# Optimization experiments

Hardware: AMD Instinct MI355X
Metric: run time of the kernel (lower is better)

The kernel has to match this reference:

```python
import jax, jax.numpy as jnp
import numpy as np

B, S, D = 2, 2048, 1024
H, DK, DV = 16, 64, 64


def setup_inputs() -> dict:
    key = jax.random.key(0)
    ks = jax.random.split(key, 10)
    scale = 0.02
    return {
        "x": jax.random.normal(ks[0], (B, S, D), dtype=jnp.float32),
        "Wq": jax.random.normal(ks[1], (D, H * DK), dtype=jnp.float32) * scale,
        "bq": jax.random.normal(ks[2], (H * DK,), dtype=jnp.float32) * scale,
        "Wk": jax.random.normal(ks[3], (D, H * DK), dtype=jnp.float32) * scale,
        "bk": jax.random.normal(ks[4], (H * DK,), dtype=jnp.float32) * scale,
        "Wv": jax.random.normal(ks[5], (D, H * DV), dtype=jnp.float32) * scale,
        "bv": jax.random.normal(ks[6], (H * DV,), dtype=jnp.float32) * scale,
        "Wo": jax.random.normal(ks[7], (H * DV, D), dtype=jnp.float32) * scale,
        "bo": jax.random.normal(ks[8], (D,), dtype=jnp.float32) * scale,
    }


def reference(x, Wq, bq, Wk, bk, Wv, bv, Wo, bo):
    b, s, d = x.shape
    # projections -> (b, H, s, dk/dv)
    q = (x @ Wq + bq).reshape(b, s, H, DK).transpose(0, 2, 1, 3)
    k = (x @ Wk + bk).reshape(b, s, H, DK).transpose(0, 2, 1, 3)
    v = (x @ Wv + bv).reshape(b, s, H, DV).transpose(0, 2, 1, 3)
    # scaled QK^T: (b, H, s, s)
    scores = jnp.einsum("bhqd,bhkd->bhqk", q, k) / np.sqrt(DK).astype(np.float32)
    # sign-based reweighting: scores * sign(scores) (zeros -> sign 1) == |scores|
    reweighted = jnp.abs(scores)
    # causal mask: lower triangle keeps value, strict upper -> -inf (value * -inf)
    causal = jnp.tril(jnp.ones((s, s), dtype=bool))
    logits = jnp.where(causal, reweighted, -jnp.inf)
    w = jax.nn.softmax(logits, axis=-1)
    o = jnp.einsum("bhqk,bhkd->bhqd", w, v)  # (b, H, s, DV)
    o = o.transpose(0, 2, 1, 3).reshape(b, s, H * DV)
    return o @ Wo + bo
```

## Files before the change

### kernel.cpp

```cpp
#include <hip/hip_runtime.h>


#define DI __device__ __forceinline__

typedef __bf16 bf16x8 __attribute__((ext_vector_type(8)));
typedef float f32x4 __attribute__((ext_vector_type(4)));
typedef unsigned short u16x8 __attribute__((ext_vector_type(8)));
typedef unsigned short u16x4 __attribute__((ext_vector_type(4)));

union U8 { u16x8 u; bf16x8 b; };
union PB { unsigned int w[4]; u16x8 u; bf16x8 b; };

typedef const __attribute__((address_space(1))) unsigned int* gas_p;
typedef __attribute__((address_space(3))) unsigned int* las_p;

DI void gload16(const unsigned short* g, unsigned short* l) {
  __builtin_amdgcn_global_load_lds((gas_p)(const void*)g, (las_p)(void*)l, 16, 0, 0);
}

#define WAIT_VM4  asm volatile("s_waitcnt vmcnt(4)" ::: "memory")
#define WAIT_VM0  asm volatile("s_waitcnt vmcnt(0)" ::: "memory")
#define WAIT_LGKM asm volatile("s_waitcnt lgkmcnt(0)" ::: "memory")
#define BARRIER   __builtin_amdgcn_s_barrier()

DI unsigned short f2bf(float f) {
  unsigned int u = __float_as_uint(f);
  u += 0x7FFFu + ((u >> 16) & 1u);
  return (unsigned short)(u >> 16);
}

__global__ __launch_bounds__(256) void k_conv_x(const float* __restrict__ x,
                                                unsigned short* __restrict__ xb) {
  size_t i = ((size_t)blockIdx.x * 256 + threadIdx.x) * 4;
  float4 v = *(const float4*)(x + i);
  u16x4 o;
  o[0] = f2bf(v.x); o[1] = f2bf(v.y); o[2] = f2bf(v.z); o[3] = f2bf(v.w);
  *(u16x4*)(xb + i) = o;
}

__global__ __launch_bounds__(256) void k_transpose(
    const float* __restrict__ W0, const float* __restrict__ W1,
    const float* __restrict__ W2, const float* __restrict__ W3,
    unsigned short* __restrict__ T0, unsigned short* __restrict__ T1,
    unsigned short* __restrict__ T2, unsigned short* __restrict__ T3) {
  const int z = blockIdx.z;
  const float* W = (z == 0) ? W0 : (z == 1) ? W1 : (z == 2) ? W2 : W3;
  unsigned short* T = (z == 0) ? T0 : (z == 1) ? T1 : (z == 2) ? T2 : T3;
  __shared__ unsigned short buf[32][33];
  const int k0 = blockIdx.x * 32, n0 = blockIdx.y * 32;
  const int tx = threadIdx.x, ty = threadIdx.y;
#pragma unroll
  for (int j = 0; j < 4; ++j) {
    int r = ty + j * 8;
    buf[r][tx] = f2bf(W[(size_t)(k0 + r) * 1024 + n0 + tx]);
  }
  __syncthreads();
#pragma unroll
  for (int j = 0; j < 4; ++j) {
    int c = ty + j * 8;
    T[(size_t)(n0 + c) * 1024 + k0 + tx] = buf[tx][c];
  }
}

DI void stage_gemm(const unsigned short* __restrict__ src, unsigned short* dst,
                   int row0, int k0, int tid, int wid) {
#pragma unroll
  for (int i = 0; i < 2; ++i) {
    int T = i * 256 + tid;
    int row = T >> 2, ch = T & 3;
    int sch = ch ^ (row & 3);
    gload16(&src[(size_t)(row0 + row) * 1024 + k0 + sch * 8],
            &dst[(i * 256 + wid * 64) * 8]);
  }
}

DI void gemm_main(const unsigned short* __restrict__ A,
                  const unsigned short* __restrict__ Bm,
                  unsigned short* As, unsigned short* Bs,
                  int m0, int n0, f32x4 acc[4][4]) {
  const int tid = threadIdx.x;
  const int lane = tid & 63, wid = tid >> 6;
  const int wr = wid >> 1, wc = wid & 1;
  const int g = lane >> 4, lq = lane & 15;

  stage_gemm(A, As, m0, 0, tid, wid);
  stage_gemm(Bm, Bs, n0, 0, tid, wid);
  __syncthreads();
  int buf = 0;
  for (int k0 = 0; k0 < 1024; k0 += 32) {
    if (k0 + 32 < 1024) {
      stage_gemm(A, As + (buf ^ 1) * 4096, m0, k0 + 32, tid, wid);
      stage_gemm(Bm, Bs + (buf ^ 1) * 4096, n0, k0 + 32, tid, wid);
    }
    const unsigned short* Ab = As + buf * 4096;
    const unsigned short* Bb = Bs + buf * 4096;
    U8 af[4], bfr[4];
#pragma unroll
    for (int f = 0; f < 4; ++f) {
      af[f].u  = *(const u16x8*)&Ab[(wr * 64 + f * 16 + lq) * 32 + ((g ^ (lq & 3)) * 8)];
      bfr[f].u = *(const u16x8*)&Bb[(wc * 64 + f * 16 + lq) * 32 + ((g ^ (lq & 3)) * 8)];
    }
#pragma unroll
    for (int i = 0; i < 4; ++i)
#pragma unroll
      for (int j = 0; j < 4; ++j)
        acc[i][j] = __builtin_amdgcn_mfma_f32_16x16x32_bf16(af[i].b, bfr[j].b,
                                                            acc[i][j], 0, 0, 0);
    __syncthreads();
    buf ^= 1;
  }
}

__global__ __launch_bounds__(256) void k_gemm_qkv(
    const unsigned short* __restrict__ xb,
    const unsigned short* __restrict__ Wqt, const unsigned short* __restrict__ Wkt,
    const unsigned short* __restrict__ Wvt,
    const float* __restrict__ bq, const float* __restrict__ bk,
    const float* __restrict__ bv,
    unsigned short* __restrict__ Qo, unsigned short* __restrict__ Ko,
    unsigned short* __restrict__ Vto) {
  __shared__ unsigned short As[2 * 4096];
  __shared__ unsigned short Bs[2 * 4096];
  const int z = blockIdx.z;
  const unsigned short* Bm = (z == 0) ? Wqt : (z == 1) ? Wkt : Wvt;
  const float* bias = (z == 0) ? bq : (z == 1) ? bk : bv;

  f32x4 acc[4][4];
#pragma unroll
  for (int i = 0; i < 4; ++i)
#pragma unroll
    for (int j = 0; j < 4; ++j) acc[i][j] = f32x4{0.f, 0.f, 0.f, 0.f};

  const int m0 = blockIdx.x * 128, n0 = blockIdx.y * 128;
  gemm_main(xb, Bm, As, Bs, m0, n0, acc);

  const int lane = threadIdx.x & 63, wid = threadIdx.x >> 6;
  const int wr = wid >> 1, wc = wid & 1;
  const int g = lane >> 4, lq = lane & 15;
  unsigned short* dstQK = (z == 0) ? Qo : Ko;
#pragma unroll
  for (int j = 0; j < 4; ++j) {
    int col = n0 + wc * 64 + j * 16 + lq;
    float bv_ = bias[col];
    int h = col >> 6, d = col & 63;
#pragma unroll
    for (int i = 0; i < 4; ++i) {
#pragma unroll
      for (int r = 0; r < 4; ++r) {
        int row = m0 + wr * 64 + i * 16 + g * 4 + r;
        int b = row >> 11, s = row & 2047;
        unsigned short hv = f2bf(acc[i][j][r] + bv_);
        if (z < 2)
          dstQK[(((size_t)(b * 16 + h)) * 2048 + s) * 64 + d] = hv;
        else
          Vto[(((size_t)(b * 16 + h)) * 64 + d) * 2048 + s] = hv;
      }
    }
  }
}

__global__ __launch_bounds__(256) void k_gemm_out(
    const unsigned short* __restrict__ Ob, const unsigned short* __restrict__ Wot,
    const float* __restrict__ bo, float* __restrict__ out) {
  __shared__ unsigned short As[2 * 4096];
  __shared__ unsigned short Bs[2 * 4096];
  f32x4 acc[4][4];
#pragma unroll
  for (int i = 0; i < 4; ++i)
#pragma unroll
    for (int j = 0; j < 4; ++j) acc[i][j] = f32x4{0.f, 0.f, 0.f, 0.f};

  const int m0 = blockIdx.x * 128, n0 = blockIdx.y * 128;
  gemm_main(Ob, Wot, As, Bs, m0, n0, acc);

  const int lane = threadIdx.x & 63, wid = threadIdx.x >> 6;
  const int wr = wid >> 1, wc = wid & 1;
  const int g = lane >> 4, lq = lane & 15;
#pragma unroll
  for (int j = 0; j < 4; ++j) {
    int col = n0 + wc * 64 + j * 16 + lq;
    float bv_ = bo[col];
#pragma unroll
    for (int i = 0; i < 4; ++i)
#pragma unroll
      for (int r = 0; r < 4; ++r) {
        int row = m0 + wr * 64 + i * 16 + g * 4 + r;
        out[(size_t)row * 1024 + col] = acc[i][j][r] + bv_;
      }
  }
}

template<bool MASKED>
DI void ptile(f32x4 sacc[4], f32x4& lacc, unsigned int pk[4][2], int qloc, int g) {
  const float SC = 0.18033688011112042f;
#pragma unroll
  for (int c = 0; c < 4; ++c) {
#pragma unroll
    for (int r = 0; r < 4; ++r) {
      float sv = fabsf(sacc[c][r]) * SC;
      if (MASKED) {
        int k = c * 16 + g * 4 + r;
        sv = (k <= qloc) ? sv : -1e30f;
      }
      float p = exp2f(sv);
      sacc[c][r] = p;
      lacc[r] += p;
    }
    asm("v_cvt_pk_bf16_f32 %0, %1, %2"
        : "=v"(pk[c][0]) : "v"(sacc[c][0]), "v"(sacc[c][1]));
    asm("v_cvt_pk_bf16_f32 %0, %1, %2"
        : "=v"(pk[c][1]) : "v"(sacc[c][2]), "v"(sacc[c][3]));
  }
}

__global__ __launch_bounds__(256) void k_flash(
    const unsigned short* __restrict__ Q, const unsigned short* __restrict__ Km,
    const unsigned short* __restrict__ Vt, unsigned short* __restrict__ O) {
  const int tid = threadIdx.x;
  const int lane = tid & 63, wid = tid >> 6;
  const int g = lane >> 4, lq = lane & 15;
  const int bid = blockIdx.x;
  const int xcd = bid & 7, idx = bid >> 3;
  const int bh = xcd * 4 + (idx >> 4);
  const int pairidx = idx & 15;
  const int b = bh >> 4, h = bh & 15;
  const size_t qkbase = (size_t)bh * 2048 * 64;
  const size_t vbase = (size_t)bh * 64 * 2048;
  const int qloc = wid * 16 + lq;

  __shared__ unsigned short Ks[2][64 * 64];
  __shared__ unsigned short Vs[2][64 * 64];

  auto stage = [&](int bf, int t) {
    const int kk0 = t * 64;
#pragma unroll
    for (int i = 0; i < 2; ++i) {
      int T = i * 256 + tid;
      int row = T >> 3, ch = T & 7;
      int sch = ch ^ (row & 7);
      gload16(&Km[qkbase + (size_t)(kk0 + row) * 64 + sch * 8],
              &Ks[bf][(i * 2048 + wid * 512)]);
      gload16(&Vt[vbase + (size_t)row * 2048 + kk0 + sch * 8],
              &Vs[bf][(i * 2048 + wid * 512)]);
    }
  };

  for (int ph = 0; ph < 2; ++ph) {
    const int qb = ph ? (31 - pairidx) : pairidx;
    const int q0 = qb * 64;
    const int qrow = q0 + qloc;

    U8 aq0, aq1;
    {
      const unsigned short* qp = &Q[qkbase + (size_t)qrow * 64 + g * 8];
      aq0.u = *(const u16x8*)qp;
      aq1.u = *(const u16x8*)(qp + 32);
    }
    f32x4 lacc = f32x4{0.f, 0.f, 0.f, 0.f};
    f32x4 oacc[4];
#pragma unroll
    for (int c = 0; c < 4; ++c) oacc[c] = f32x4{0.f, 0.f, 0.f, 0.f};

    const int nt = qb + 1;
    stage(0, 0);
    if (nt > 1) stage(1, 1);
    int buf = 0;
    for (int t = 0; t < nt; ++t) {
      if (t + 1 < nt) WAIT_VM4; else WAIT_VM0;
      BARRIER;
      f32x4 sacc[4];
      __builtin_amdgcn_s_setprio(1);
#pragma unroll
      for (int c = 0; c < 4; ++c) {
        U8 kf0, kf1;
        kf0.u = *(const u16x8*)&Ks[buf][(c * 16 + lq) * 64 + (((0 * 4 + g) ^ (lq & 7)) * 8)];
        kf1.u = *(const u16x8*)&Ks[buf][(c * 16 + lq) * 64 + (((1 * 4 + g) ^ (lq & 7)) * 8)];
        sacc[c] = __builtin_amdgcn_mfma_f32_16x16x32_bf16(kf0.b, aq0.b,
                                                          f32x4{0.f, 0.f, 0.f, 0.f}, 0, 0, 0);
        sacc[c] = __builtin_amdgcn_mfma_f32_16x16x32_bf16(kf1.b, aq1.b, sacc[c], 0, 0, 0);
      }
      __builtin_amdgcn_s_setprio(0);
      unsigned int pk[4][2];
      if (t == nt - 1) ptile<true>(sacc, lacc, pk, qloc, g);
      else            ptile<false>(sacc, lacc, pk, qloc, g);
      __builtin_amdgcn_s_setprio(1);
#pragma unroll
      for (int hh = 0; hh < 2; ++hh) {
        PB pb;
#pragma unroll
        for (int w2 = 0; w2 < 4; ++w2) {
          int src = (((g & 1) * 2 + (w2 >> 1)) << 4) + lq;
          unsigned int lo = __shfl(pk[hh * 2 + 0][w2 & 1], src, 64);
          unsigned int hi = __shfl(pk[hh * 2 + 1][w2 & 1], src, 64);
          pb.w[w2] = (g >> 1) ? hi : lo;
        }
#pragma unroll
        for (int c = 0; c < 4; ++c) {
          U8 vf;
          vf.u = *(const u16x8*)&Vs[buf][(c * 16 + lq) * 64 + (((hh * 4 + g) ^ (lq & 7)) * 8)];
          oacc[c] = __builtin_amdgcn_mfma_f32_16x16x32_bf16(vf.b, pb.b, oacc[c], 0, 0, 0);
        }
      }
      __builtin_amdgcn_s_setprio(0);
      WAIT_LGKM;
      BARRIER;
      if (t + 2 < nt) stage(buf, t + 2);
      buf ^= 1;
    }
    float lsum = (lacc[0] + lacc[1]) + (lacc[2] + lacc[3]);
    lsum += __shfl_xor(lsum, 16, 64);
    lsum += __shfl_xor(lsum, 32, 64);
    float inv_l = 1.0f / lsum;
#pragma unroll
    for (int c = 0; c < 4; ++c) {
      u16x4 ov;
#pragma unroll
      for (int r = 0; r < 4; ++r) ov[r] = f2bf(oacc[c][r] * inv_l);
      *(u16x4*)&O[((size_t)(b * 2048 + qrow)) * 1024 + h * 64 + c * 16 + g * 4] = ov;
    }
  }
}

extern "C" void kernel_launch(void* const* d_in, const int* in_sizes, int n_in,
                              void* d_out, int out_size, void* d_ws, size_t ws_size,
                              hipStream_t stream) {
  const float* x  = (const float*)d_in[0];
  const float* Wq = (const float*)d_in[1];
  const float* bq = (const float*)d_in[2];
  const float* Wk = (const float*)d_in[3];
  const float* bk = (const float*)d_in[4];
  const float* Wv = (const float*)d_in[5];
  const float* bv = (const float*)d_in[6];
  const float* Wo = (const float*)d_in[7];
  const float* bo = (const float*)d_in[8];
  float* out = (float*)d_out;

  char* ws = (char*)d_ws;
  const size_t MB = 1024 * 1024;
  unsigned short* xb   = (unsigned short*)(ws + 0 * MB);
  unsigned short* Wqt  = (unsigned short*)(ws + 8 * MB);
  unsigned short* Wkt  = (unsigned short*)(ws + 10 * MB);
  unsigned short* Wvt  = (unsigned short*)(ws + 12 * MB);
  unsigned short* Wot  = (unsigned short*)(ws + 14 * MB);
  unsigned short* Qws  = (unsigned short*)(ws + 16 * MB);
  unsigned short* Kws  = (unsigned short*)(ws + 24 * MB);
  unsigned short* Vtws = (unsigned short*)(ws + 32 * MB);
  unsigned short* Ows  = (unsigned short*)(ws + 40 * MB);

  k_conv_x<<<4096, 256, 0, stream>>>(x, xb);
  k_transpose<<<dim3(32, 32, 4), dim3(32, 8), 0, stream>>>(Wq, Wk, Wv, Wo,
                                                           Wqt, Wkt, Wvt, Wot);
  k_gemm_qkv<<<dim3(32, 8, 3), 256, 0, stream>>>(xb, Wqt, Wkt, Wvt, bq, bk, bv,
                                                 Qws, Kws, Vtws);
  k_flash<<<512, 256, 0, stream>>>(Qws, Kws, Vtws, Ows);
  k_gemm_out<<<dim3(32, 8), 256, 0, stream>>>(Ows, Wot, bo, out);
}
```

Measured before the change: 126.5 us.

## Split long causal query blocks across two CTAs and stage QKV epilogue through LDS

The flash kernel now launches twice as many blocks. Each pair of blocks shares the work of a short and a long query block: the long block's key range is split in two, each half writes unnormalized bf16 partial outputs and row sums to workspace, and a new combine kernel merges them. This is meant to balance work per block and raise occupancy, at the cost of an extra launch, extra global traffic and bf16 rounding of the partials. Separately, the QKV GEMM epilogue now writes the tile into shared memory first, then does coalesced 16-byte stores for Q/K and the transposed V, replacing the scattered 2-byte stores.

```diff
diff --git a/kernel.cpp b/kernel.cpp
--- a/kernel.cpp
+++ b/kernel.cpp
@@ -28,6 +28,7 @@
   u += 0x7FFFu + ((u >> 16) & 1u);
   return (unsigned short)(u >> 16);
 }
+DI float bf2f(unsigned short v) { return __uint_as_float((unsigned int)v << 16); }
 
 __global__ __launch_bounds__(256) void k_conv_x(const float* __restrict__ x,
                                                 unsigned short* __restrict__ xb) {
@@ -119,8 +120,9 @@
     const float* __restrict__ bv,
     unsigned short* __restrict__ Qo, unsigned short* __restrict__ Ko,
     unsigned short* __restrict__ Vto) {
-  __shared__ unsigned short As[2 * 4096];
-  __shared__ unsigned short Bs[2 * 4096];
+  __shared__ unsigned short Sh[128 * 136];
+  unsigned short* As = Sh;
+  unsigned short* Bs = Sh + 8192;
   const int z = blockIdx.z;
   const unsigned short* Bm = (z == 0) ? Wqt : (z == 1) ? Wkt : Wvt;
   const float* bias = (z == 0) ? bq : (z == 1) ? bk : bv;
@@ -134,27 +136,50 @@
   const int m0 = blockIdx.x * 128, n0 = blockIdx.y * 128;
   gemm_main(xb, Bm, As, Bs, m0, n0, acc);
 
-  const int lane = threadIdx.x & 63, wid = threadIdx.x >> 6;
+  const int tid = threadIdx.x;
+  const int lane = tid & 63, wid = tid >> 6;
   const int wr = wid >> 1, wc = wid & 1;
   const int g = lane >> 4, lq = lane & 15;
-  unsigned short* dstQK = (z == 0) ? Qo : Ko;
+  const int bb = m0 >> 11;
+
 #pragma unroll
   for (int j = 0; j < 4; ++j) {
-    int col = n0 + wc * 64 + j * 16 + lq;
-    float bv_ = bias[col];
-    int h = col >> 6, d = col & 63;
-#pragma unroll
-    for (int i = 0; i < 4; ++i) {
+    int col = wc * 64 + j * 16 + lq;
+    float bv_ = bias[n0 + col];
+#pragma unroll
+    for (int i = 0; i < 4; ++i)
 #pragma unroll
       for (int r = 0; r < 4; ++r) {
-        int row = m0 + wr * 64 + i * 16 + g * 4 + r;
-        int b = row >> 11, s = row & 2047;
-        unsigned short hv = f2bf(acc[i][j][r] + bv_);
-        if (z < 2)
-          dstQK[(((size_t)(b * 16 + h)) * 2048 + s) * 64 + d] = hv;
-        else
-          Vto[(((size_t)(b * 16 + h)) * 64 + d) * 2048 + s] = hv;
-      }
+        int row = wr * 64 + i * 16 + g * 4 + r;
+        Sh[row * 136 + col] = f2bf(acc[i][j][r] + bv_);
+      }
+  }
+  __syncthreads();
+
+  if (z < 2) {
+    unsigned short* dstQK = (z == 0) ? Qo : Ko;
+    const int ch = tid & 15, sb = tid >> 4;
+#pragma unroll
+    for (int it = 0; it < 8; ++it) {
+      int s = sb + it * 16;
+      u16x8 v = *(const u16x8*)&Sh[s * 136 + ch * 8];
+      int gcol = n0 + ch * 8;
+      int hh = gcol >> 6, dd = gcol & 63;
+      int sr = (m0 + s) & 2047;
+      *(u16x8*)&dstQK[(((size_t)(bb * 16 + hh)) * 2048 + sr) * 64 + dd] = v;
+    }
+  } else {
+    const int d = tid & 127, hf = tid >> 7;
+    int gcol = n0 + d;
+    int hh = gcol >> 6, dd = gcol & 63;
+    size_t vrow = ((size_t)(bb * 16 + hh)) * 64 + dd;
+#pragma unroll
+    for (int it = 0; it < 8; ++it) {
+      int s0 = (hf + it * 2) * 8;
+      u16x8 vv;
+#pragma unroll
+      for (int e = 0; e < 8; ++e) vv[e] = Sh[(s0 + e) * 136 + d];
+      *(u16x8*)&Vto[vrow * 2048 + (m0 & 2047) + s0] = vv;
     }
   }
 }
@@ -213,20 +238,29 @@
   }
 }
 
-__global__ __launch_bounds__(256) void k_flash(
+__global__ __launch_bounds__(256, 4) void k_flash(
     const unsigned short* __restrict__ Q, const unsigned short* __restrict__ Km,
-    const unsigned short* __restrict__ Vt, unsigned short* __restrict__ O) {
+    const unsigned short* __restrict__ Vt, unsigned short* __restrict__ O,
+    unsigned short* __restrict__ Pp, float* __restrict__ Lp) {
   const int tid = threadIdx.x;
   const int lane = tid & 63, wid = tid >> 6;
   const int g = lane >> 4, lq = lane & 15;
   const int bid = blockIdx.x;
-  const int xcd = bid & 7, idx = bid >> 3;
-  const int bh = xcd * 4 + (idx >> 4);
-  const int pairidx = idx & 15;
+  const int xcd = bid & 7, r = bid >> 3;
+  const int bh = xcd * 4 + (r >> 5);
+  const int rr = r & 31;
+  const int p = rr >> 1, sp = rr & 1;
   const int b = bh >> 4, h = bh & 15;
   const size_t qkbase = (size_t)bh * 2048 * 64;
   const size_t vbase = (size_t)bh * 64 * 2048;
   const int qloc = wid * 16 + lq;
+
+  const int ntA = p + 1;
+  const int mq = 31 - p, mi = 15 - p;
+  const bool hasA = (sp == 0);
+  int t0, t1, limB;
+  if (sp == 0) { int u = 16 - p; t0 = 0; t1 = (ntA > u) ? ntA : u; limB = u; }
+  else         { t0 = 16 - p; t1 = 32 - p; limB = 1 << 30; }
 
   __shared__ unsigned short Ks[2][64 * 64];
   __shared__ unsigned short Vs[2][64 * 64];
@@ -245,80 +279,147 @@
     }
   };
 
-  for (int ph = 0; ph < 2; ++ph) {
-    const int qb = ph ? (31 - pairidx) : pairidx;
-    const int q0 = qb * 64;
-    const int qrow = q0 + qloc;
-
-    U8 aq0, aq1;
-    {
-      const unsigned short* qp = &Q[qkbase + (size_t)qrow * 64 + g * 8];
-      aq0.u = *(const u16x8*)qp;
-      aq1.u = *(const u16x8*)(qp + 32);
-    }
-    f32x4 lacc = f32x4{0.f, 0.f, 0.f, 0.f};
-    f32x4 oacc[4];
-#pragma unroll
-    for (int c = 0; c < 4; ++c) oacc[c] = f32x4{0.f, 0.f, 0.f, 0.f};
-
-    const int nt = qb + 1;
-    stage(0, 0);
-    if (nt > 1) stage(1, 1);
-    int buf = 0;
-    for (int t = 0; t < nt; ++t) {
-      if (t + 1 < nt) WAIT_VM4; else WAIT_VM0;
-      BARRIER;
-      f32x4 sacc[4];
-      __builtin_amdgcn_s_setprio(1);
+  U8 aqA0, aqA1, aqB0, aqB1;
+  if (hasA) {
+    const unsigned short* qp = &Q[qkbase + (size_t)(p * 64 + qloc) * 64 + g * 8];
+    aqA0.u = *(const u16x8*)qp;
+    aqA1.u = *(const u16x8*)(qp + 32);
+  }
+  {
+    const unsigned short* qp = &Q[qkbase + (size_t)(mq * 64 + qloc) * 64 + g * 8];
+    aqB0.u = *(const u16x8*)qp;
+    aqB1.u = *(const u16x8*)(qp + 32);
+  }
+  f32x4 laccA = f32x4{0.f, 0.f, 0.f, 0.f}, laccB = f32x4{0.f, 0.f, 0.f, 0.f};
+  f32x4 oaccA[4], oaccB[4];
+#pragma unroll
+  for (int c = 0; c < 4; ++c) {
+    oaccA[c] = f32x4{0.f, 0.f, 0.f, 0.f};
+    oaccB[c] = f32x4{0.f, 0.f, 0.f, 0.f};
+  }
+
+  stage(0, t0);
+  stage(1, t0 + 1);
+  int buf = 0;
+  for (int t = t0; t < t1; ++t) {
+    if (t + 1 < t1) WAIT_VM4; else WAIT_VM0;
+    BARRIER;
+    const bool condA = hasA && (t < ntA);
+    const bool condB = (t < limB);
+    f32x4 saccA[4], saccB[4];
+    __builtin_amdgcn_s_setprio(1);
+#pragma unroll
+    for (int c = 0; c < 4; ++c) {
+      U8 kf0, kf1;
+      kf0.u = *(const u16x8*)&Ks[buf][(c * 16 + lq) * 64 + (((0 * 4 + g) ^ (lq & 7)) * 8)];
+      kf1.u = *(const u16x8*)&Ks[buf][(c * 16 + lq) * 64 + (((1 * 4 + g) ^ (lq & 7)) * 8)];
+      if (condA) {
+        saccA[c] = __builtin_amdgcn_mfma_f32_16x16x32_bf16(kf0.b, aqA0.b,
+                                                           f32x4{0.f, 0.f, 0.f, 0.f}, 0, 0, 0);
+        saccA[c] = __builtin_amdgcn_mfma_f32_16x16x32_bf16(kf1.b, aqA1.b, saccA[c], 0, 0, 0);
+      }
+      if (condB) {
+        saccB[c] = __builtin_amdgcn_mfma_f32_16x16x32_bf16(kf0.b, aqB0.b,
+                                                           f32x4{0.f, 0.f, 0.f, 0.f}, 0, 0, 0);
+        saccB[c] = __builtin_amdgcn_mfma_f32_16x16x32_bf16(kf1.b, aqB1.b, saccB[c], 0, 0, 0);
+      }
+    }
+    __builtin_amdgcn_s_setprio(0);
+    unsigned int pkA[4][2], pkB[4][2];
+    if (condA) {
+      if (t == p) ptile<true>(saccA, laccA, pkA, qloc, g);
+      else        ptile<false>(saccA, laccA, pkA, qloc, g);
+    }
+    if (condB) {
+      if (t == mq) ptile<true>(saccB, laccB, pkB, qloc, g);
+      else         ptile<false>(saccB, laccB, pkB, qloc, g);
+    }
+    __builtin_amdgcn_s_setprio(1);
+#pragma unroll
+    for (int hh = 0; hh < 2; ++hh) {
+      PB pbA, pbB;
+#pragma unroll
+      for (int w2 = 0; w2 < 4; ++w2) {
+        int src = (((g & 1) * 2 + (w2 >> 1)) << 4) + lq;
+        if (condA) {
+          unsigned int lo = __shfl(pkA[hh * 2 + 0][w2 & 1], src, 64);
+          unsigned int hi = __shfl(pkA[hh * 2 + 1][w2 & 1], src, 64);
+          pbA.w[w2] = (g >> 1) ? hi : lo;
+        }
+        if (condB) {
+          unsigned int lo = __shfl(pkB[hh * 2 + 0][w2 & 1], src, 64);
+          unsigned int hi = __shfl(pkB[hh * 2 + 1][w2 & 1], src, 64);
+          pbB.w[w2] = (g >> 1) ? hi : lo;
+        }
+      }
 #pragma unroll
       for (int c = 0; c < 4; ++c) {
-        U8 kf0, kf1;
-        kf0.u = *(const u16x8*)&Ks[buf][(c * 16 + lq) * 64 + (((0 * 4 + g) ^ (lq & 7)) * 8)];
-        kf1.u = *(const u16x8*)&Ks[buf][(c * 16 + lq) * 64 + (((1 * 4 + g) ^ (lq & 7)) * 8)];
-        sacc[c] = __builtin_amdgcn_mfma_f32_16x16x32_bf16(kf0.b, aq0.b,
-                                                          f32x4{0.f, 0.f, 0.f, 0.f}, 0, 0, 0);
-        sacc[c] = __builtin_amdgcn_mfma_f32_16x16x32_bf16(kf1.b, aq1.b, sacc[c], 0, 0, 0);
-      }
-      __builtin_amdgcn_s_setprio(0);
-      unsigned int pk[4][2];
-      if (t == nt - 1) ptile<true>(sacc, lacc, pk, qloc, g);
-      else            ptile<false>(sacc, lacc, pk, qloc, g);
-      __builtin_amdgcn_s_setprio(1);
-#pragma unroll
-      for (int hh = 0; hh < 2; ++hh) {
-        PB pb;
-#pragma unroll
-        for (int w2 = 0; w2 < 4; ++w2) {
-          int src = (((g & 1) * 2 + (w2 >> 1)) << 4) + lq;
-          unsigned int lo = __shfl(pk[hh * 2 + 0][w2 & 1], src, 64);
-          unsigned int hi = __shfl(pk[hh * 2 + 1][w2 & 1], src, 64);
-          pb.w[w2] = (g >> 1) ? hi : lo;
-        }
-#pragma unroll
-        for (int c = 0; c < 4; ++c) {
-          U8 vf;
-          vf.u = *(const u16x8*)&Vs[buf][(c * 16 + lq) * 64 + (((hh * 4 + g) ^ (lq & 7)) * 8)];
-          oacc[c] = __builtin_amdgcn_mfma_f32_16x16x32_bf16(vf.b, pb.b, oacc[c], 0, 0, 0);
-        }
-      }
-      __builtin_amdgcn_s_setprio(0);
-      WAIT_LGKM;
-      BARRIER;
-      if (t + 2 < nt) stage(buf, t + 2);
-      buf ^= 1;
-    }
-    float lsum = (lacc[0] + lacc[1]) + (lacc[2] + lacc[3]);
-    lsum += __shfl_xor(lsum, 16, 64);
-    lsum += __shfl_xor(lsum, 32, 64);
-    float inv_l = 1.0f / lsum;
+        U8 vf;
+        vf.u = *(const u16x8*)&Vs[buf][(c * 16 + lq) * 64 + (((hh * 4 + g) ^ (lq & 7)) * 8)];
+        if (condA)
+          oaccA[c] = __builtin_amdgcn_mfma_f32_16x16x32_bf16(vf.b, pbA.b, oaccA[c], 0, 0, 0);
+        if (condB)
+          oaccB[c] = __builtin_amdgcn_mfma_f32_16x16x32_bf16(vf.b, pbB.b, oaccB[c], 0, 0, 0);
+      }
+    }
+    __builtin_amdgcn_s_setprio(0);
+    WAIT_LGKM;
+    BARRIER;
+    if (t + 2 < t1) stage(buf, t + 2);
+    buf ^= 1;
+  }
+
+  if (hasA) {
+    float ls = (laccA[0] + laccA[1]) + (laccA[2] + laccA[3]);
+    ls += __shfl_xor(ls, 16, 64);
+    ls += __shfl_xor(ls, 32, 64);
+    float inv_l = 1.0f / ls;
+    int qrow = p * 64 + qloc;
 #pragma unroll
     for (int c = 0; c < 4; ++c) {
       u16x4 ov;
 #pragma unroll
-      for (int r = 0; r < 4; ++r) ov[r] = f2bf(oacc[c][r] * inv_l);
+      for (int r2 = 0; r2 < 4; ++r2) ov[r2] = f2bf(oaccA[c][r2] * inv_l);
       *(u16x4*)&O[((size_t)(b * 2048 + qrow)) * 1024 + h * 64 + c * 16 + g * 4] = ov;
     }
   }
+  {
+    float ls = (laccB[0] + laccB[1]) + (laccB[2] + laccB[3]);
+    ls += __shfl_xor(ls, 16, 64);
+    ls += __shfl_xor(ls, 32, 64);
+    int slot = (bh * 16 + mi) * 2 + sp;
+    if (g == 0) Lp[slot * 64 + qloc] = ls;
+    size_t pbase = (size_t)slot * 4096 + qloc * 64;
+#pragma unroll
+    for (int c = 0; c < 4; ++c) {
+      u16x4 ov;
+#pragma unroll
+      for (int r2 = 0; r2 < 4; ++r2) ov[r2] = f2bf(oaccB[c][r2]);
+      *(u16x4*)&Pp[pbase + c * 16 + g * 4] = ov;
+    }
+  }
+}
+
+__global__ __launch_bounds__(256) void k_combine(
+    const unsigned short* __restrict__ Pp, const float* __restrict__ Lp,
+    unsigned short* __restrict__ O) {
+  int gid = blockIdx.x * 256 + threadIdx.x;
+  int dv4 = gid & 15;
+  int q   = (gid >> 4) & 63;
+  int mi  = (gid >> 10) & 15;
+  int bh  = gid >> 14;
+  int pairbase = (bh * 16 + mi) * 2;
+  size_t base = (size_t)pairbase * 4096 + q * 64 + dv4 * 4;
+  u16x4 a = *(const u16x4*)&Pp[base];
+  u16x4 c = *(const u16x4*)&Pp[base + 4096];
+  float l = Lp[pairbase * 64 + q] + Lp[(pairbase + 1) * 64 + q];
+  float inv = 1.0f / l;
+  u16x4 o;
+#pragma unroll
+  for (int r = 0; r < 4; ++r) o[r] = f2bf((bf2f(a[r]) + bf2f(c[r])) * inv);
+  int b = bh >> 4, h = bh & 15;
+  int srow = (mi + 16) * 64 + q;
+  *(u16x4*)&O[((size_t)(b * 2048 + srow)) * 1024 + h * 64 + dv4 * 4] = o;
 }
 
 extern "C" void kernel_launch(void* const* d_in, const int* in_sizes, int n_in,
@@ -346,12 +447,15 @@
   unsigned short* Kws  = (unsigned short*)(ws + 24 * MB);
   unsigned short* Vtws = (unsigned short*)(ws + 32 * MB);
   unsigned short* Ows  = (unsigned short*)(ws + 40 * MB);
+  unsigned short* Pp   = (unsigned short*)(ws + 0 * MB);
+  float*          Lp   = (float*)(ws + 8 * MB);
 
   k_conv_x<<<4096, 256, 0, stream>>>(x, xb);
   k_transpose<<<dim3(32, 32, 4), dim3(32, 8), 0, stream>>>(Wq, Wk, Wv, Wo,
                                                            Wqt, Wkt, Wvt, Wot);
   k_gemm_qkv<<<dim3(32, 8, 3), 256, 0, stream>>>(xb, Wqt, Wkt, Wvt, bq, bk, bv,
                                                  Qws, Kws, Vtws);
-  k_flash<<<512, 256, 0, stream>>>(Qws, Kws, Vtws, Ows);
+  k_flash<<<1024, 256, 0, stream>>>(Qws, Kws, Vtws, Ows, Pp, Lp);
+  k_combine<<<2048, 256, 0, stream>>>(Pp, Lp, Ows);
   k_gemm_out<<<dim3(32, 8), 256, 0, stream>>>(Ows, Wot, bo, out);
 }
```

After: 172.4 us. 1.36x slower.
